# Performance work log

Measured on AMD Instinct MI355X. Metric: run time of the kernel, lower is better.

The kernel has to match this reference:

```python
import math
import jax, jax.numpy as jnp
import numpy as np

H = 1024        # hidden_size
NH = 16         # num_attention_heads
HD = H // NH    # attention_head_size
I = 4096        # intermediate_size
B, S = 4, 2048
LN_EPS = 1e-5


def setup_inputs() -> dict:
    key = jax.random.key(0)
    ks = jax.random.split(key, 12)
    s = 0.02
    return {
        "x": jax.random.normal(ks[0], (B, S, H), dtype=jnp.float32),
        "ln1_g": jnp.ones((H,), jnp.float32),
        "ln1_b": jnp.zeros((H,), jnp.float32),
        "qkv_w": jax.random.normal(ks[1], (H, 3 * H), jnp.float32) * s,
        "qkv_b": jnp.zeros((3 * H,), jnp.float32),
        "out_w": jax.random.normal(ks[2], (H, H), jnp.float32) * s,
        "out_b": jnp.zeros((H,), jnp.float32),
        "ln2_g": jnp.ones((H,), jnp.float32),
        "ln2_b": jnp.zeros((H,), jnp.float32),
        "w1": jax.random.normal(ks[3], (H, I), jnp.float32) * s,
        "b1": jnp.zeros((I,), jnp.float32),
        "w2": jax.random.normal(ks[4], (I, H), jnp.float32) * s,
        "b2": jnp.zeros((H,), jnp.float32),
    }


def _layernorm(x, g, b):
    mu = jnp.mean(x, axis=-1, keepdims=True)
    var = jnp.mean(jnp.square(x - mu), axis=-1, keepdims=True)
    return (x - mu) * jax.lax.rsqrt(var + LN_EPS) * g + b


def _gelu_tanh(x):
    c = math.sqrt(2.0 / math.pi)
    return 0.5 * x * (1.0 + jnp.tanh(c * (x + 0.044715 * x * x * x)))


def reference(x, ln1_g, ln1_b, qkv_w, qkv_b, out_w, out_b, ln2_g, ln2_b, w1, b1, w2, b2):
    b, s, _ = x.shape
    h = _layernorm(x, ln1_g, ln1_b)
    qkv = h @ qkv_w + qkv_b                      # [B,S,3H]
    q, k, v = jnp.split(qkv, 3, axis=-1)
    # [B,S,H] -> [B,NH,S,HD]
    def heads(t):
        return t.reshape(b, s, NH, HD).transpose(0, 2, 1, 3)
    q, k, v = heads(q), heads(k), heads(v)
    scores = jnp.einsum("bhqd,bhkd->bhqk", q, k) / math.sqrt(HD)
    probs = jax.nn.softmax(scores, axis=-1)
    attn = jnp.einsum("bhqk,bhkd->bhqd", probs, v)
    attn = attn.transpose(0, 2, 1, 3).reshape(b, s, H)
    attn = attn @ out_w + out_b
    x = x + attn
    h2 = _layernorm(x, ln2_g, ln2_b)
    mlp = _gelu_tanh(h2 @ w1 + b1) @ w2 + b2
    x = x + mlp
    return x
```

## Files before the change

### kernel.cpp

```cpp
#include <hip/hip_runtime.h>
#include <math.h>

#define H 1024
#define NHEAD 16
#define HDIM 64
#define IDIM 4096
#define BATCH 4
#define SEQ 2048
#define NTOK 8192
#define LN_EPS 1e-5f

#define QK_EXP2_SCALE 0.18033688011112042f

typedef __bf16 bf16x8 __attribute__((ext_vector_type(8)));
typedef __bf16 bf16x4 __attribute__((ext_vector_type(4)));
typedef float f32x4 __attribute__((ext_vector_type(4)));
typedef unsigned short ushort8 __attribute__((ext_vector_type(8)));
typedef unsigned short ushort4v __attribute__((ext_vector_type(4)));

__device__ __forceinline__ unsigned short f2bf(float f) {
  union { float f; unsigned int u; } v; v.f = f;
  unsigned int u = v.u;
  return (unsigned short)((u + 0x7FFFu + ((u >> 16) & 1u)) >> 16);
}

__global__ void transpose_cast_kernel(const float* __restrict__ W,
                                      unsigned short* __restrict__ Wt,
                                      int K, int N) {
  __shared__ unsigned short tile[32][33];
  int n0 = blockIdx.x * 32, k0 = blockIdx.y * 32;
  int tx = threadIdx.x, ty = threadIdx.y;
#pragma unroll
  for (int i = 0; i < 4; i++) {
    int k = ty + i * 8;
    tile[tx][k] = f2bf(W[(size_t)(k0 + k) * N + n0 + tx]);
  }
  __syncthreads();
#pragma unroll
  for (int i = 0; i < 4; i++) {
    int n = ty + i * 8;
    Wt[(size_t)(n0 + n) * K + k0 + tx] = tile[n][tx];
  }
}

__global__ __launch_bounds__(256)
void layernorm_kernel(const float* __restrict__ x, const float* __restrict__ g,
                      const float* __restrict__ b, unsigned short* __restrict__ out) {
  __shared__ float sb[4];
  int row = blockIdx.x;
  int tid = threadIdx.x;
  const float4* xr = (const float4*)(x + (size_t)row * H);
  float4 v = xr[tid];
  float s = v.x + v.y + v.z + v.w;
#pragma unroll
  for (int o = 32; o > 0; o >>= 1) s += __shfl_down(s, o);
  if ((tid & 63) == 0) sb[tid >> 6] = s;
  __syncthreads();
  float mu = (sb[0] + sb[1] + sb[2] + sb[3]) * (1.0f / H);
  __syncthreads();
  float dx = v.x - mu, dy = v.y - mu, dz = v.z - mu, dw = v.w - mu;
  float s2 = dx * dx + dy * dy + dz * dz + dw * dw;
#pragma unroll
  for (int o = 32; o > 0; o >>= 1) s2 += __shfl_down(s2, o);
  if ((tid & 63) == 0) sb[tid >> 6] = s2;
  __syncthreads();
  float var = (sb[0] + sb[1] + sb[2] + sb[3]) * (1.0f / H);
  float rs = rsqrtf(var + LN_EPS);
  float4 gv = ((const float4*)g)[tid];
  float4 bv = ((const float4*)b)[tid];
  ushort4v ov;
  ov[0] = f2bf(dx * rs * gv.x + bv.x);
  ov[1] = f2bf(dy * rs * gv.y + bv.y);
  ov[2] = f2bf(dz * rs * gv.z + bv.z);
  ov[3] = f2bf(dw * rs * gv.w + bv.w);
  ((ushort4v*)(out + (size_t)row * H))[tid] = ov;
}

template <int EPI>
__global__ __launch_bounds__(256)
void gemm_bt_kernel(const unsigned short* __restrict__ A,
                    const unsigned short* __restrict__ Bt,
                    const float* __restrict__ bias,
                    const float* __restrict__ res,
                    void* __restrict__ out, unsigned short* __restrict__ vt_out,
                    int M, int N, int K) {
  __shared__ __align__(16) unsigned short As[2][128 * 32];
  __shared__ __align__(16) unsigned short Bs[2][128 * 32];
  int tid = threadIdx.x;
  int wave = tid >> 6, lane = tid & 63;
  int quad = lane >> 4, l16 = lane & 15;
  int wm = wave >> 1, wn = wave & 1;
  int m0 = blockIdx.y * 128, n0 = blockIdx.x * 128;
  f32x4 acc[4][4];
#pragma unroll
  for (int i = 0; i < 4; i++)
#pragma unroll
    for (int j = 0; j < 4; j++) acc[i][j] = (f32x4){0.f, 0.f, 0.f, 0.f};

  int rl = (lane >> 2);
  int cphys = lane & 3;

  auto stage = [&](int k0, int sel) {
#pragma unroll
    for (int t = 0; t < 2; t++) {
      int ch = wave * 2 + t;
      int rloc = ch * 16 + rl;
      int clog = cphys ^ ((rloc >> 1) & 3);
      const unsigned short* ga = A + (size_t)(m0 + rloc) * K + k0 + clog * 8;
      __builtin_amdgcn_global_load_lds(
          (const __attribute__((address_space(1))) unsigned int*)ga,
          (__attribute__((address_space(3))) unsigned int*)(&As[sel][ch * 512]), 16, 0, 0);
      const unsigned short* gb = Bt + (size_t)(n0 + rloc) * K + k0 + clog * 8;
      __builtin_amdgcn_global_load_lds(
          (const __attribute__((address_space(1))) unsigned int*)gb,
          (__attribute__((address_space(3))) unsigned int*)(&Bs[sel][ch * 512]), 16, 0, 0);
    }
  };

  stage(0, 0);
  for (int k0 = 0; k0 < K; k0 += 32) {
    int sel = (k0 >> 5) & 1;
    __syncthreads();
    if (k0 + 32 < K) stage(k0 + 32, sel ^ 1);
    bf16x8 af[4], bfv[4];
#pragma unroll
    for (int i = 0; i < 4; i++) {
      int ra = wm * 64 + i * 16 + l16;
      af[i] = *(const bf16x8*)&As[sel][ra * 32 + ((quad ^ ((ra >> 1) & 3)) << 3)];
      int rb = wn * 64 + i * 16 + l16;
      bfv[i] = *(const bf16x8*)&Bs[sel][rb * 32 + ((quad ^ ((rb >> 1) & 3)) << 3)];
    }
#pragma unroll
    for (int i = 0; i < 4; i++)
#pragma unroll
      for (int j = 0; j < 4; j++)
        acc[i][j] = __builtin_amdgcn_mfma_f32_16x16x32_bf16(bfv[j], af[i], acc[i][j], 0, 0, 0);
  }
  bool vslice = (EPI == 0) && (vt_out != nullptr) && (n0 >= 2 * H);
#pragma unroll
  for (int i = 0; i < 4; i++) {
    int m = m0 + wm * 64 + i * 16 + l16;
#pragma unroll
    for (int j = 0; j < 4; j++) {
      int nb = n0 + wn * 64 + j * 16 + quad * 4;
      float4 bv4 = *(const float4*)&bias[nb];
      float v0 = acc[i][j][0] + bv4.x;
      float v1 = acc[i][j][1] + bv4.y;
      float v2 = acc[i][j][2] + bv4.z;
      float v3 = acc[i][j][3] + bv4.w;
      size_t off = (size_t)m * N + nb;
      if (EPI == 0) {
        if (vslice) {
          int bb = m >> 11, s = m & (SEQ - 1);
          int cb = nb - 2 * H;
          int hh = cb >> 6, dd = cb & 63;
          size_t base = ((size_t)(bb * NHEAD + hh) * HDIM + dd) * SEQ + s;
          vt_out[base] = f2bf(v0);
          vt_out[base + SEQ] = f2bf(v1);
          vt_out[base + 2 * SEQ] = f2bf(v2);
          vt_out[base + 3 * SEQ] = f2bf(v3);
        } else {
          if (n0 < H) {
            v0 *= QK_EXP2_SCALE; v1 *= QK_EXP2_SCALE;
            v2 *= QK_EXP2_SCALE; v3 *= QK_EXP2_SCALE;
          }
          bf16x4 pk = {(__bf16)v0, (__bf16)v1, (__bf16)v2, (__bf16)v3};
          *(bf16x4*)&((unsigned short*)out)[off] = pk;
        }
      } else if (EPI == 1) {
        float g0 = v0 / (1.f + __expf(-1.5957691216057308f * (v0 + 0.044715f * v0 * v0 * v0)));
        float g1 = v1 / (1.f + __expf(-1.5957691216057308f * (v1 + 0.044715f * v1 * v1 * v1)));
        float g2 = v2 / (1.f + __expf(-1.5957691216057308f * (v2 + 0.044715f * v2 * v2 * v2)));
        float g3 = v3 / (1.f + __expf(-1.5957691216057308f * (v3 + 0.044715f * v3 * v3 * v3)));
        bf16x4 pk = {(__bf16)g0, (__bf16)g1, (__bf16)g2, (__bf16)g3};
        *(bf16x4*)&((unsigned short*)out)[off] = pk;
      } else {
        float4 rv = *(const float4*)&res[off];
        float4 o4;
        o4.x = v0 + rv.x; o4.y = v1 + rv.y; o4.z = v2 + rv.z; o4.w = v3 + rv.w;
        *(float4*)&((float*)out)[off] = o4;
      }
    }
  }
}

__global__ __launch_bounds__(512, 4)
void flash_attn_kernel(const unsigned short* __restrict__ qkv,
                       const unsigned short* __restrict__ vt,
                       unsigned short* __restrict__ attn_out) {
  constexpr int LPs = 40;
  __shared__ __align__(16) unsigned short Ks[2][64 * 64];
  __shared__ __align__(16) unsigned short Ps[8 * 32 * LPs];
  int tid = threadIdx.x;
  int wave = tid >> 6, lane = tid & 63;
  int quad = lane >> 4, l16 = lane & 15;
  int d = blockIdx.x;
  int logical = (d & 7) * 64 + (d >> 3);
  int bh = logical >> 3, qi = logical & 7;
  int b = bh >> 4, h = bh & 15;
  int qblk = qi * 256 + wave * 32;
  const size_t qrow = 3 * H;
  const size_t tok0 = (size_t)b * SEQ;
  const size_t vbase = (size_t)bh * HDIM * SEQ;
  unsigned short* Psw = Ps + wave * 32 * LPs;

  bf16x8 qb[2][2];
#pragma unroll
  for (int mb = 0; mb < 2; mb++)
#pragma unroll
    for (int ks = 0; ks < 2; ks++)
      qb[mb][ks] = *(const bf16x8*)&qkv[(tok0 + qblk + mb * 16 + l16) * qrow +
                                        h * HDIM + ks * 32 + quad * 8];

  float l_part[2] = {0.f, 0.f};
  f32x4 o_acc[2][4];
#pragma unroll
  for (int mb = 0; mb < 2; mb++)
#pragma unroll
    for (int db = 0; db < 4; db++) o_acc[mb][db] = (f32x4){0.f, 0.f, 0.f, 0.f};

  int srow = lane >> 3;
  int schunk = (lane & 7) ^ srow;

  {
    const unsigned short* ga =
        &qkv[(tok0 + wave * 8 + srow) * qrow + H + h * HDIM + schunk * 8];
    __builtin_amdgcn_global_load_lds(
        (const __attribute__((address_space(1))) unsigned int*)ga,
        (__attribute__((address_space(3))) unsigned int*)(&Ks[0][wave * 8 * 64]), 16, 0, 0);
  }

  for (int kv0 = 0; kv0 < SEQ; kv0 += 64) {
    int buf = (kv0 >> 6) & 1;
    const unsigned short* Kb = Ks[buf];
    unsigned short* Kn = Ks[buf ^ 1];
    __syncthreads();
    bf16x8 va[4];
#pragma unroll
    for (int db = 0; db < 4; db++)
      va[db] = *(const bf16x8*)&vt[vbase + (size_t)(db * 16 + l16) * SEQ +
                                   kv0 + quad * 8];
    if (kv0 + 64 < SEQ) {
      const unsigned short* ga =
          &qkv[(tok0 + kv0 + 64 + wave * 8 + srow) * qrow + H + h * HDIM + schunk * 8];
      __builtin_amdgcn_global_load_lds(
          (const __attribute__((address_space(1))) unsigned int*)ga,
          (__attribute__((address_space(3))) unsigned int*)(Kn + wave * 8 * 64), 16, 0, 0);
    }
#pragma unroll
    for (int half = 0; half < 2; half++) {
#pragma unroll
      for (int nbl = 0; nbl < 2; nbl++) {
        int nb = half * 2 + nbl;
        int row = nb * 16 + l16;
        bf16x8 ka[2];
#pragma unroll
        for (int ks = 0; ks < 2; ks++) {
          int pc = (ks * 4 + quad) ^ (row & 7);
          ka[ks] = *(const bf16x8*)&Kb[row * 64 + pc * 8];
        }
        f32x4 st[2];
#pragma unroll
        for (int mb = 0; mb < 2; mb++) st[mb] = (f32x4){0.f, 0.f, 0.f, 0.f};
        __builtin_amdgcn_s_setprio(1);
#pragma unroll
        for (int ks = 0; ks < 2; ks++)
#pragma unroll
          for (int mb = 0; mb < 2; mb++)
            st[mb] = __builtin_amdgcn_mfma_f32_16x16x32_bf16(ka[ks], qb[mb][ks], st[mb], 0, 0, 0);
        __builtin_amdgcn_s_setprio(0);
#pragma unroll
        for (int mb = 0; mb < 2; mb++) {
          float p0, p1, p2, p3;
          asm("v_exp_f32 %0, %1" : "=v"(p0) : "v"(st[mb][0]));
          asm("v_exp_f32 %0, %1" : "=v"(p1) : "v"(st[mb][1]));
          asm("v_exp_f32 %0, %1" : "=v"(p2) : "v"(st[mb][2]));
          asm("v_exp_f32 %0, %1" : "=v"(p3) : "v"(st[mb][3]));
          l_part[mb] += (p0 + p1) + (p2 + p3);
          bf16x4 pk = {(__bf16)p0, (__bf16)p1, (__bf16)p2, (__bf16)p3};
          *(bf16x4*)&Psw[(mb * 16 + l16) * LPs + nb * 16 + quad * 4] = pk;
        }
      }
      __asm__ volatile("s_waitcnt lgkmcnt(0)" ::: "memory");
      bf16x8 pb[2];
#pragma unroll
      for (int mb = 0; mb < 2; mb++)
        pb[mb] = *(const bf16x8*)&Psw[(mb * 16 + l16) * LPs + half * 32 + quad * 8];
      __builtin_amdgcn_s_setprio(1);
#pragma unroll
      for (int db = 0; db < 4; db++)
#pragma unroll
        for (int mb = 0; mb < 2; mb++)
          o_acc[mb][db] = __builtin_amdgcn_mfma_f32_16x16x32_bf16(va[db], pb[mb],
                                                                  o_acc[mb][db], 0, 0, 0);
      __builtin_amdgcn_s_setprio(0);
      if (half == 0) {
#pragma unroll
        for (int db = 0; db < 4; db++)
          va[db] = *(const bf16x8*)&vt[vbase + (size_t)(db * 16 + l16) * SEQ +
                                       kv0 + 32 + quad * 8];
      }
    }
  }
#pragma unroll
  for (int mb = 0; mb < 2; mb++) {
    l_part[mb] += __shfl_xor(l_part[mb], 16);
    l_part[mb] += __shfl_xor(l_part[mb], 32);
    l_part[mb] = 1.0f / l_part[mb];
  }
#pragma unroll
  for (int mb = 0; mb < 2; mb++) {
#pragma unroll
    for (int db = 0; db < 4; db++) {
      ushort4v o;
#pragma unroll
      for (int r = 0; r < 4; r++) o[r] = f2bf(o_acc[mb][db][r] * l_part[mb]);
      *(ushort4v*)&attn_out[(tok0 + qblk + mb * 16 + l16) * H + h * HDIM +
                            db * 16 + quad * 4] = o;
    }
  }
}

extern "C" void kernel_launch(void* const* d_in, const int* in_sizes, int n_in,
                              void* d_out, int out_size, void* d_ws, size_t ws_size,
                              hipStream_t stream) {
  const float* x = (const float*)d_in[0];
  const float* ln1_g = (const float*)d_in[1];
  const float* ln1_b = (const float*)d_in[2];
  const float* qkv_w = (const float*)d_in[3];
  const float* qkv_b = (const float*)d_in[4];
  const float* out_w = (const float*)d_in[5];
  const float* out_b = (const float*)d_in[6];
  const float* ln2_g = (const float*)d_in[7];
  const float* ln2_b = (const float*)d_in[8];
  const float* w1 = (const float*)d_in[9];
  const float* b1 = (const float*)d_in[10];
  const float* w2 = (const float*)d_in[11];
  const float* b2 = (const float*)d_in[12];
  float* outp = (float*)d_out;

  size_t off = 0;
  auto take = [&](size_t n) {
    char* p = (char*)d_ws + off;
    off += (n + 255) & ~(size_t)255;
    return p;
  };
  unsigned short* h1 = (unsigned short*)take((size_t)NTOK * H * 2);
  unsigned short* qkvb = (unsigned short*)take((size_t)NTOK * 3 * H * 2);
  unsigned short* attn = (unsigned short*)take((size_t)NTOK * H * 2);
  float* x1 = (float*)take((size_t)NTOK * H * 4);
  unsigned short* qkvwt = (unsigned short*)take((size_t)3 * H * H * 2);
  unsigned short* outwt = (unsigned short*)take((size_t)H * H * 2);
  unsigned short* w1t = (unsigned short*)take((size_t)H * IDIM * 2);
  unsigned short* w2t = (unsigned short*)take((size_t)H * IDIM * 2);
  unsigned short* h2 = h1;
  unsigned short* mid = qkvb;
  unsigned short* vt = (unsigned short*)x1;

  dim3 tb(32, 8);
  transpose_cast_kernel<<<dim3(3 * H / 32, H / 32), tb, 0, stream>>>(qkv_w, qkvwt, H, 3 * H);
  transpose_cast_kernel<<<dim3(H / 32, H / 32), tb, 0, stream>>>(out_w, outwt, H, H);
  transpose_cast_kernel<<<dim3(IDIM / 32, H / 32), tb, 0, stream>>>(w1, w1t, H, IDIM);
  transpose_cast_kernel<<<dim3(H / 32, IDIM / 32), tb, 0, stream>>>(w2, w2t, IDIM, H);

  layernorm_kernel<<<NTOK, 256, 0, stream>>>(x, ln1_g, ln1_b, h1);
  gemm_bt_kernel<0><<<dim3(3 * H / 128, NTOK / 128), 256, 0, stream>>>(
      h1, qkvwt, qkv_b, nullptr, qkvb, vt, NTOK, 3 * H, H);
  flash_attn_kernel<<<dim3(SEQ / 256 * BATCH * NHEAD), 512, 0, stream>>>(qkvb, vt, attn);
  gemm_bt_kernel<2><<<dim3(H / 128, NTOK / 128), 256, 0, stream>>>(
      attn, outwt, out_b, x, x1, nullptr, NTOK, H, H);
  layernorm_kernel<<<NTOK, 256, 0, stream>>>(x1, ln2_g, ln2_b, h2);
  gemm_bt_kernel<1><<<dim3(IDIM / 128, NTOK / 128), 256, 0, stream>>>(
      h2, w1t, b1, nullptr, mid, nullptr, NTOK, IDIM, H);
  gemm_bt_kernel<2><<<dim3(H / 128, NTOK / 128), 256, 0, stream>>>(
      mid, w2t, b2, x1, outp, nullptr, NTOK, H, IDIM);
}
```

Baseline: 611.3 us.

## Add 256x256 pipelined GEMM kernel for QKV and FFN1 projections

```diff
diff --git a/kernel.cpp b/kernel.cpp
--- a/kernel.cpp
+++ b/kernel.cpp
@@ -136,10 +136,160 @@
       for (int j = 0; j < 4; j++)
         acc[i][j] = __builtin_amdgcn_mfma_f32_16x16x32_bf16(bfv[j], af[i], acc[i][j], 0, 0, 0);
   }
-  bool vslice = (EPI == 0) && (vt_out != nullptr) && (n0 >= 2 * H);
 #pragma unroll
   for (int i = 0; i < 4; i++) {
     int m = m0 + wm * 64 + i * 16 + l16;
+#pragma unroll
+    for (int j = 0; j < 4; j++) {
+      int nb = n0 + wn * 64 + j * 16 + quad * 4;
+      float4 bv4 = *(const float4*)&bias[nb];
+      float v0 = acc[i][j][0] + bv4.x;
+      float v1 = acc[i][j][1] + bv4.y;
+      float v2 = acc[i][j][2] + bv4.z;
+      float v3 = acc[i][j][3] + bv4.w;
+      size_t off = (size_t)m * N + nb;
+      float4 rv = *(const float4*)&res[off];
+      float4 o4;
+      o4.x = v0 + rv.x; o4.y = v1 + rv.y; o4.z = v2 + rv.z; o4.w = v3 + rv.w;
+      *(float4*)&((float*)out)[off] = o4;
+    }
+  }
+}
+
+template <int EPI>
+__global__ __launch_bounds__(512, 2)
+void gemm256_kernel(const unsigned short* __restrict__ A,
+                    const unsigned short* __restrict__ Bt,
+                    const float* __restrict__ bias,
+                    void* __restrict__ out, unsigned short* __restrict__ vt_out,
+                    int M, int N, int K) {
+  __shared__ __align__(16) unsigned short As[2][256 * 64];
+  __shared__ __align__(16) unsigned short Bs[2][256 * 64];
+  int tid = threadIdx.x;
+  int wave = tid >> 6, lane = tid & 63;
+  int quad = lane >> 4, l16 = lane & 15;
+  int wm = wave >> 2, wn = wave & 3;
+  int nwg = gridDim.x * gridDim.y;
+  int dlin = blockIdx.y * gridDim.x + blockIdx.x;
+  int swz = (dlin & 7) * (nwg >> 3) + (dlin >> 3);
+  int nm = gridDim.y;
+  int mt = swz % nm, nt = swz / nm;
+  int m0 = mt * 256, n0 = nt * 256;
+  int NT = K >> 6;
+
+  const unsigned short* Abase = A + (size_t)m0 * K;
+  const unsigned short* Bbase = Bt + (size_t)n0 * K;
+
+  int srow = lane >> 3;
+  int schunk = (lane & 7) ^ srow;
+
+  auto stage = [&](const unsigned short* gbase, unsigned short* lbase, int tile,
+                   int half) {
+    int kt = tile < NT ? tile : NT - 1;
+    int k0 = kt << 6;
+    unsigned short* lb = lbase + (size_t)(tile & 1) * (256 * 64);
+#pragma unroll
+    for (int L = 0; L < 2; L++) {
+      int rloc = half * 128 + L * 64 + wave * 8 + srow;
+      const unsigned short* g = gbase + (size_t)rloc * K + k0 + schunk * 8;
+      __builtin_amdgcn_global_load_lds(
+          (const __attribute__((address_space(1))) unsigned int*)g,
+          (__attribute__((address_space(3))) unsigned int*)(lb + (size_t)(half * 128 + L * 64 + wave * 8) * 64),
+          16, 0, 0);
+    }
+  };
+
+  f32x4 acc[8][4];
+#pragma unroll
+  for (int i = 0; i < 8; i++)
+#pragma unroll
+    for (int j = 0; j < 4; j++) acc[i][j] = (f32x4){0.f, 0.f, 0.f, 0.f};
+  bf16x8 af[4][2];
+  bf16x8 bv[4][2];
+
+  stage(Abase, (unsigned short*)As, 0, 0);
+  stage(Bbase, (unsigned short*)Bs, 0, 0);
+  stage(Abase, (unsigned short*)As, 0, 1);
+  stage(Bbase, (unsigned short*)Bs, 0, 1);
+  stage(Abase, (unsigned short*)As, 1, 0);
+  stage(Bbase, (unsigned short*)Bs, 1, 0);
+  stage(Abase, (unsigned short*)As, 1, 1);
+  stage(Bbase, (unsigned short*)Bs, 1, 1);
+  asm volatile("s_waitcnt vmcnt(8)" ::: "memory");
+  __builtin_amdgcn_s_barrier();
+
+  for (int it = 0; it < (NT >> 1); it++) {
+    int t = it * 2;
+#pragma unroll
+    for (int P = 0; P < 8; P++) {
+      int ct = t + (P >> 2);
+      int sel = ct & 1;
+      if ((P & 3) == 0) {
+#pragma unroll
+        for (int i = 0; i < 4; i++) {
+          int ra = wm * 128 + i * 16 + l16;
+#pragma unroll
+          for (int ks = 0; ks < 2; ks++)
+            af[i][ks] = *(const bf16x8*)&As[sel][ra * 64 + (((ks * 4 + quad) ^ (ra & 7)) << 3)];
+        }
+#pragma unroll
+        for (int j = 0; j < 2; j++) {
+          int rb = wn * 64 + j * 16 + l16;
+#pragma unroll
+          for (int ks = 0; ks < 2; ks++)
+            bv[j][ks] = *(const bf16x8*)&Bs[sel][rb * 64 + (((ks * 4 + quad) ^ (rb & 7)) << 3)];
+        }
+      } else if ((P & 3) == 1) {
+#pragma unroll
+        for (int j = 0; j < 2; j++) {
+          int rb = wn * 64 + (2 + j) * 16 + l16;
+#pragma unroll
+          for (int ks = 0; ks < 2; ks++)
+            bv[2 + j][ks] = *(const bf16x8*)&Bs[sel][rb * 64 + (((ks * 4 + quad) ^ (rb & 7)) << 3)];
+        }
+      } else if ((P & 3) == 2) {
+#pragma unroll
+        for (int i = 0; i < 4; i++) {
+          int ra = wm * 128 + (4 + i) * 16 + l16;
+#pragma unroll
+          for (int ks = 0; ks < 2; ks++)
+            af[i][ks] = *(const bf16x8*)&As[sel][ra * 64 + (((ks * 4 + quad) ^ (ra & 7)) << 3)];
+        }
+      }
+      switch (P) {
+        case 2: stage(Bbase, (unsigned short*)Bs, t + 2, 0); break;
+        case 3: stage(Abase, (unsigned short*)As, t + 2, 0);
+                stage(Bbase, (unsigned short*)Bs, t + 2, 1); break;
+        case 4: stage(Abase, (unsigned short*)As, t + 2, 1); break;
+        case 6: stage(Bbase, (unsigned short*)Bs, t + 3, 0);
+                stage(Bbase, (unsigned short*)Bs, t + 3, 1); break;
+        case 7: stage(Abase, (unsigned short*)As, t + 3, 0);
+                stage(Abase, (unsigned short*)As, t + 3, 1); break;
+        default: break;
+      }
+      __builtin_amdgcn_s_barrier();
+      int qm = (P >> 1) & 1, qj = P & 1;
+      __builtin_amdgcn_s_setprio(1);
+#pragma unroll
+      for (int i = 0; i < 4; i++)
+#pragma unroll
+        for (int j = 0; j < 2; j++)
+#pragma unroll
+          for (int ks = 0; ks < 2; ks++)
+            acc[qm * 4 + i][qj * 2 + j] = __builtin_amdgcn_mfma_f32_16x16x32_bf16(
+                bv[qj * 2 + j][ks], af[i][ks], acc[qm * 4 + i][qj * 2 + j], 0, 0, 0);
+      __builtin_amdgcn_s_setprio(0);
+      if (P == 3) asm volatile("s_waitcnt vmcnt(6)" ::: "memory");
+      if (P == 7) asm volatile("s_waitcnt vmcnt(8)" ::: "memory");
+      __builtin_amdgcn_s_barrier();
+    }
+  }
+  asm volatile("s_waitcnt vmcnt(0)" ::: "memory");
+
+  bool vslice = (EPI == 0) && (vt_out != nullptr) && (n0 >= 2 * H);
+#pragma unroll
+  for (int i = 0; i < 8; i++) {
+    int m = m0 + wm * 128 + i * 16 + l16;
 #pragma unroll
     for (int j = 0; j < 4; j++) {
       int nb = n0 + wn * 64 + j * 16 + quad * 4;
@@ -167,18 +317,13 @@
           bf16x4 pk = {(__bf16)v0, (__bf16)v1, (__bf16)v2, (__bf16)v3};
           *(bf16x4*)&((unsigned short*)out)[off] = pk;
         }
-      } else if (EPI == 1) {
+      } else {
         float g0 = v0 / (1.f + __expf(-1.5957691216057308f * (v0 + 0.044715f * v0 * v0 * v0)));
         float g1 = v1 / (1.f + __expf(-1.5957691216057308f * (v1 + 0.044715f * v1 * v1 * v1)));
         float g2 = v2 / (1.f + __expf(-1.5957691216057308f * (v2 + 0.044715f * v2 * v2 * v2)));
         float g3 = v3 / (1.f + __expf(-1.5957691216057308f * (v3 + 0.044715f * v3 * v3 * v3)));
         bf16x4 pk = {(__bf16)g0, (__bf16)g1, (__bf16)g2, (__bf16)g3};
         *(bf16x4*)&((unsigned short*)out)[off] = pk;
-      } else {
-        float4 rv = *(const float4*)&res[off];
-        float4 o4;
-        o4.x = v0 + rv.x; o4.y = v1 + rv.y; o4.z = v2 + rv.z; o4.w = v3 + rv.w;
-        *(float4*)&((float*)out)[off] = o4;
       }
     }
   }
@@ -364,14 +509,14 @@
   transpose_cast_kernel<<<dim3(H / 32, IDIM / 32), tb, 0, stream>>>(w2, w2t, IDIM, H);
 
   layernorm_kernel<<<NTOK, 256, 0, stream>>>(x, ln1_g, ln1_b, h1);
-  gemm_bt_kernel<0><<<dim3(3 * H / 128, NTOK / 128), 256, 0, stream>>>(
-      h1, qkvwt, qkv_b, nullptr, qkvb, vt, NTOK, 3 * H, H);
+  gemm256_kernel<0><<<dim3(3 * H / 256, NTOK / 256), 512, 0, stream>>>(
+      h1, qkvwt, qkv_b, qkvb, vt, NTOK, 3 * H, H);
   flash_attn_kernel<<<dim3(SEQ / 256 * BATCH * NHEAD), 512, 0, stream>>>(qkvb, vt, attn);
   gemm_bt_kernel<2><<<dim3(H / 128, NTOK / 128), 256, 0, stream>>>(
       attn, outwt, out_b, x, x1, nullptr, NTOK, H, H);
   layernorm_kernel<<<NTOK, 256, 0, stream>>>(x1, ln2_g, ln2_b, h2);
-  gemm_bt_kernel<1><<<dim3(IDIM / 128, NTOK / 128), 256, 0, stream>>>(
-      h2, w1t, b1, nullptr, mid, nullptr, NTOK, IDIM, H);
+  gemm256_kernel<1><<<dim3(IDIM / 256, NTOK / 256), 512, 0, stream>>>(
+      h2, w1t, b1, mid, nullptr, NTOK, IDIM, H);
   gemm_bt_kernel<2><<<dim3(H / 128, NTOK / 128), 256, 0, stream>>>(
       mid, w2t, b2, x1, outp, nullptr, NTOK, H, IDIM);
 }
```

New measurement: 607.9 us. No clear change (-0.6%).
